# Performance work log

Measured on AMD Instinct MI355X. Metric: run time of the kernel, lower is better.

## Reference

```python
import jax, jax.numpy as jnp
import numpy as np

SEQ, BATCH, IN_DIM, NQ = 512, 512, 128, 8  # hidden_dim == n_qubits == 8


def setup_inputs() -> dict:
    key = jax.random.key(0)
    k1, k2, k3, k4 = jax.random.split(key, 4)
    inputs = jax.random.normal(k1, (SEQ, BATCH, IN_DIM), dtype=jnp.float32)
    h0 = jnp.zeros((BATCH, NQ), dtype=jnp.float32)
    c0 = jnp.zeros((BATCH, NQ), dtype=jnp.float32)
    D = IN_DIM + NQ
    # gate order: forget, input, update, output
    W = jax.random.normal(k2, (4, NQ, D), dtype=jnp.float32) / np.sqrt(D)
    b = jnp.zeros((4, NQ), dtype=jnp.float32)
    qp = jax.random.normal(k3, (4, NQ), dtype=jnp.float32)  # QLayer.params per gate
    return {"inputs": inputs, "h0": h0, "c0": c0, "W": W, "b": b, "qp": qp}


def _qlayer(z):
    # Analytic form of the RY/RY/CNOT-chain circuit: <Z_k> = prod_{j<=k} cos(theta_j)
    return jnp.cumprod(jnp.cos(z), axis=-1)


def reference(inputs, h0, c0, W, b, qp):
    def step(carry, x_t):
        h, c = carry
        comb = jnp.concatenate([x_t, h], axis=-1)            # (B, D)
        z = jnp.einsum('bd,gqd->bgq', comb, W) + b + qp      # (B, 4, NQ)
        q = _qlayer(z)
        f = jax.nn.sigmoid(q[:, 0])
        i = jax.nn.sigmoid(q[:, 1])
        g = jnp.tanh(q[:, 2])
        o = jax.nn.sigmoid(q[:, 3])
        c2 = f * c + i * g
        h2 = o * jnp.tanh(c2)
        return (h2, c2), h2

    (h_f, c_f), outputs = jax.lax.scan(step, (h0, c0), inputs)
    return outputs, h_f, c_f
```

## Files before the change

kernel.cpp:

```cpp
#include <hip/hip_runtime.h>


#define SEQ_LEN 512
#define BATCH_N 512
#define IN_DIMC 128
#define NQC 8
#define DTOT 136
#define GQ 32
#define M_ROWS (SEQ_LEN * BATCH_N)
#define OUT_MAIN (SEQ_LEN * BATCH_N * NQC)

__global__ __launch_bounds__(256) void zx_gemm(
    const float* __restrict__ X, const float* __restrict__ W,
    float* __restrict__ ZX)
{
    __shared__ __align__(16) float Wl[IN_DIMC * GQ];
    const int tid = threadIdx.x;

    #pragma unroll
    for (int i = 0; i < (IN_DIMC * GQ) / 256; ++i) {
        int idx = i * 256 + tid;
        int k  = idx >> 5;
        int gq = idx & 31;
        Wl[idx] = W[gq * DTOT + k];
    }
    __syncthreads();

    const float4* __restrict__ X4  = (const float4*)X;
    const float4* __restrict__ Wl4 = (const float4*)Wl;

    const int r0 = blockIdx.x * 512 + tid;
    const int r1 = r0 + 256;

    float4 accA[8], accB[8];
    #pragma unroll
    for (int q = 0; q < 8; ++q) {
        accA[q] = make_float4(0.f, 0.f, 0.f, 0.f);
        accB[q] = make_float4(0.f, 0.f, 0.f, 0.f);
    }

#define KSTEP(XA, XB, KIDX)                                                   \
    {                                                                         \
        _Pragma("unroll")                                                     \
        for (int q = 0; q < 8; ++q) {                                         \
            float4 w = Wl4[(KIDX) * 8 + q];                                   \
            accA[q].x = fmaf((XA), w.x, accA[q].x);                           \
            accA[q].y = fmaf((XA), w.y, accA[q].y);                           \
            accA[q].z = fmaf((XA), w.z, accA[q].z);                           \
            accA[q].w = fmaf((XA), w.w, accA[q].w);                           \
            accB[q].x = fmaf((XB), w.x, accB[q].x);                           \
            accB[q].y = fmaf((XB), w.y, accB[q].y);                           \
            accB[q].z = fmaf((XB), w.z, accB[q].z);                           \
            accB[q].w = fmaf((XB), w.w, accB[q].w);                           \
        }                                                                     \
    }

    #pragma unroll 2
    for (int k4 = 0; k4 < 32; ++k4) {
        float4 xa = X4[r0 * 32 + k4];
        float4 xb = X4[r1 * 32 + k4];
        KSTEP(xa.x, xb.x, k4 * 4 + 0)
        KSTEP(xa.y, xb.y, k4 * 4 + 1)
        KSTEP(xa.z, xb.z, k4 * 4 + 2)
        KSTEP(xa.w, xb.w, k4 * 4 + 3)
    }
#undef KSTEP

    float4* __restrict__ Z4 = (float4*)ZX;
    #pragma unroll
    for (int q = 0; q < 8; ++q) {
        Z4[r0 * 8 + q] = accA[q];
        Z4[r1 * 8 + q] = accB[q];
    }
}

__device__ __forceinline__ float fast_rcp(float x) {
    return __builtin_amdgcn_rcpf(x);
}
__device__ __forceinline__ float sigmoid_f(float x) {
    return fast_rcp(1.f + __expf(-x));
}
__device__ __forceinline__ float tanh_f(float x) {
    return fmaf(2.f, fast_rcp(1.f + __expf(-2.f * x)), -1.f);
}

__global__ __launch_bounds__(64) void qlstm_scan(
    const float* __restrict__ ZX, const float* __restrict__ W,
    const float* __restrict__ bv, const float* __restrict__ qp,
    const float* __restrict__ h0, const float* __restrict__ c0,
    float* __restrict__ out)
{
    const int tid = threadIdx.x;
    const int l32 = tid & 31;
    const int hw  = tid >> 5;
    const int qi  = l32 & 7;
    const int gq  = l32;
    const int row = blockIdx.x * 2 + hw;

    float wh[8];
    #pragma unroll
    for (int j = 0; j < 8; ++j) wh[j] = W[gq * DTOT + IN_DIMC + j];
    const float bias = bv[gq] + qp[gq];

    float hreg[8];
    #pragma unroll
    for (int j = 0; j < 8; ++j) hreg[j] = h0[row * 8 + j];
    float c = c0[row * 8 + qi];

    float zcur = ZX[(long)row * 32 + l32];

    float h2 = 0.f;
    for (int t = 0; t < SEQ_LEN; ++t) {
        const int tn = (t + 1 < SEQ_LEN) ? (t + 1) : (SEQ_LEN - 1);
        const float znext = ZX[((long)tn * BATCH_N + row) * 32 + l32];

        float z = zcur + bias;
        #pragma unroll
        for (int j = 0; j < 8; ++j) z = fmaf(hreg[j], wh[j], z);

        float p = __cosf(z);
        #pragma unroll
        for (int off = 1; off <= 4; off <<= 1) {
            int src = (qi >= off) ? (l32 - off) : l32;
            float pv = __shfl(p, src, 32);
            p = (qi >= off) ? p * pv : p;
        }

        float p0 = __shfl(p, qi,      32);
        float p1 = __shfl(p, qi + 8,  32);
        float p2 = __shfl(p, qi + 16, 32);
        float p3 = __shfl(p, qi + 24, 32);

        float fg = sigmoid_f(p0);
        float ig = sigmoid_f(p1);
        float gg = tanh_f(p2);
        float og = sigmoid_f(p3);

        float c2 = fmaf(fg, c, ig * gg);
        h2 = og * tanh_f(c2);
        c = c2;

        #pragma unroll
        for (int j = 0; j < 8; ++j) hreg[j] = __shfl(h2, j, 32);

        if (l32 < 8)
            out[((long)t * BATCH_N + row) * 8 + qi] = h2;

        zcur = znext;
    }

    if (l32 < 8) {
        out[OUT_MAIN + row * 8 + qi] = h2;
        out[OUT_MAIN + BATCH_N * NQC + row * 8 + qi] = c;
    }
}

extern "C" void kernel_launch(void* const* d_in, const int* in_sizes, int n_in,
                              void* d_out, int out_size, void* d_ws, size_t ws_size,
                              hipStream_t stream)
{
    const float* X  = (const float*)d_in[0];
    const float* h0 = (const float*)d_in[1];
    const float* c0 = (const float*)d_in[2];
    const float* W  = (const float*)d_in[3];
    const float* bv = (const float*)d_in[4];
    const float* qp = (const float*)d_in[5];
    float* out = (float*)d_out;
    float* ZX  = (float*)d_ws;

    zx_gemm<<<M_ROWS / 512, 256, 0, stream>>>(X, W, ZX);
    qlstm_scan<<<BATCH_N / 2, 64, 0, stream>>>(ZX, W, bv, qp, h0, c0, out);
}
```

Baseline: 420.4 us.

## Pack four rows per wave with DPP exchanges and fold bias into GEMM

The scan kernel now maps 16 lanes per batch row instead of 32, with each lane computing two gate pre-activations. It replaces ds_bpermute shuffles with DPP row rotations and shifts for the cumprod scan, the gate exchange and the h broadcast, and prefetches ZX two steps ahead. Bias plus qp is folded into the GEMM epilogue, and the GEMM loop gets explicit one-step X prefetch with unroll 1. The goal is to shorten the serial per-step latency chain and halve the number of waves. The cost is more math per lane and DPP direction handling (dirshr), which is fragile.

```diff
diff --git a/kernel.cpp b/kernel.cpp
--- a/kernel.cpp
+++ b/kernel.cpp
@@ -4,154 +4,208 @@
 #define SEQ_LEN 512
 #define BATCH_N 512
 #define IN_DIMC 128
-#define NQC 8
 #define DTOT 136
-#define GQ 32
-#define M_ROWS (SEQ_LEN * BATCH_N)
-#define OUT_MAIN (SEQ_LEN * BATCH_N * NQC)
+#define OUT_MAIN (SEQ_LEN * BATCH_N * 8)
 
 __global__ __launch_bounds__(256) void zx_gemm(
     const float* __restrict__ X, const float* __restrict__ W,
+    const float* __restrict__ bv, const float* __restrict__ qp,
     float* __restrict__ ZX)
 {
-    __shared__ __align__(16) float Wl[IN_DIMC * GQ];
+    __shared__ __align__(16) float Wl[IN_DIMC * 32];
     const int tid = threadIdx.x;
-
-    #pragma unroll
-    for (int i = 0; i < (IN_DIMC * GQ) / 256; ++i) {
+    #pragma unroll
+    for (int i = 0; i < 16; ++i) {
         int idx = i * 256 + tid;
-        int k  = idx >> 5;
-        int gq = idx & 31;
-        Wl[idx] = W[gq * DTOT + k];
+        Wl[idx] = W[(idx & 31) * DTOT + (idx >> 5)];
     }
     __syncthreads();
 
-    const float4* __restrict__ X4  = (const float4*)X;
-    const float4* __restrict__ Wl4 = (const float4*)Wl;
-
-    const int r0 = blockIdx.x * 512 + tid;
-    const int r1 = r0 + 256;
-
-    float4 accA[8], accB[8];
-    #pragma unroll
-    for (int q = 0; q < 8; ++q) {
-        accA[q] = make_float4(0.f, 0.f, 0.f, 0.f);
-        accB[q] = make_float4(0.f, 0.f, 0.f, 0.f);
-    }
-
-#define KSTEP(XA, XB, KIDX)                                                   \
-    {                                                                         \
-        _Pragma("unroll")                                                     \
-        for (int q = 0; q < 8; ++q) {                                         \
-            float4 w = Wl4[(KIDX) * 8 + q];                                   \
-            accA[q].x = fmaf((XA), w.x, accA[q].x);                           \
-            accA[q].y = fmaf((XA), w.y, accA[q].y);                           \
-            accA[q].z = fmaf((XA), w.z, accA[q].z);                           \
-            accA[q].w = fmaf((XA), w.w, accA[q].w);                           \
-            accB[q].x = fmaf((XB), w.x, accB[q].x);                           \
-            accB[q].y = fmaf((XB), w.y, accB[q].y);                           \
-            accB[q].z = fmaf((XB), w.z, accB[q].z);                           \
-            accB[q].w = fmaf((XB), w.w, accB[q].w);                           \
-        }                                                                     \
-    }
-
-    #pragma unroll 2
+    const long r0 = (long)blockIdx.x * 512 + tid;
+    const long r1 = r0 + 256;
+    const float4* __restrict__ X40 = (const float4*)X + r0 * 32;
+    const float4* __restrict__ X41 = (const float4*)X + r1 * 32;
+    const float4* __restrict__ W4  = (const float4*)Wl;
+
+    float4 a0[8], a1[8];
+    #pragma unroll
+    for (int qq = 0; qq < 8; ++qq) {
+        a0[qq] = make_float4(0.f, 0.f, 0.f, 0.f);
+        a1[qq] = make_float4(0.f, 0.f, 0.f, 0.f);
+    }
+
+    float4 xa = X40[0], xb = X41[0];
+    #pragma unroll 1
     for (int k4 = 0; k4 < 32; ++k4) {
-        float4 xa = X4[r0 * 32 + k4];
-        float4 xb = X4[r1 * 32 + k4];
-        KSTEP(xa.x, xb.x, k4 * 4 + 0)
-        KSTEP(xa.y, xb.y, k4 * 4 + 1)
-        KSTEP(xa.z, xb.z, k4 * 4 + 2)
-        KSTEP(xa.w, xb.w, k4 * 4 + 3)
-    }
-#undef KSTEP
+        float4 xan = xa, xbn = xb;
+        if (k4 < 31) { xan = X40[k4 + 1]; xbn = X41[k4 + 1]; }
+        #pragma unroll
+        for (int c = 0; c < 4; ++c) {
+            const float va = (c==0)?xa.x:(c==1)?xa.y:(c==2)?xa.z:xa.w;
+            const float vb = (c==0)?xb.x:(c==1)?xb.y:(c==2)?xb.z:xb.w;
+            #pragma unroll
+            for (int qq = 0; qq < 8; ++qq) {
+                const float4 w = W4[(k4 * 4 + c) * 8 + qq];
+                a0[qq].x = fmaf(va, w.x, a0[qq].x);
+                a0[qq].y = fmaf(va, w.y, a0[qq].y);
+                a0[qq].z = fmaf(va, w.z, a0[qq].z);
+                a0[qq].w = fmaf(va, w.w, a0[qq].w);
+                a1[qq].x = fmaf(vb, w.x, a1[qq].x);
+                a1[qq].y = fmaf(vb, w.y, a1[qq].y);
+                a1[qq].z = fmaf(vb, w.z, a1[qq].z);
+                a1[qq].w = fmaf(vb, w.w, a1[qq].w);
+            }
+        }
+        xa = xan; xb = xbn;
+    }
 
     float4* __restrict__ Z4 = (float4*)ZX;
     #pragma unroll
-    for (int q = 0; q < 8; ++q) {
-        Z4[r0 * 8 + q] = accA[q];
-        Z4[r1 * 8 + q] = accB[q];
+    for (int qq = 0; qq < 8; ++qq) {
+        const int g0 = qq * 4;
+        float4 o0 = a0[qq], o1 = a1[qq];
+        const float b0 = bv[g0+0] + qp[g0+0];
+        const float b1_ = bv[g0+1] + qp[g0+1];
+        const float b2 = bv[g0+2] + qp[g0+2];
+        const float b3 = bv[g0+3] + qp[g0+3];
+        o0.x += b0; o0.y += b1_; o0.z += b2; o0.w += b3;
+        o1.x += b0; o1.y += b1_; o1.z += b2; o1.w += b3;
+        Z4[r0 * 8 + qq] = o0;
+        Z4[r1 * 8 + qq] = o1;
     }
 }
 
-__device__ __forceinline__ float fast_rcp(float x) {
-    return __builtin_amdgcn_rcpf(x);
-}
-__device__ __forceinline__ float sigmoid_f(float x) {
-    return fast_rcp(1.f + __expf(-x));
-}
-__device__ __forceinline__ float tanh_f(float x) {
-    return fmaf(2.f, fast_rcp(1.f + __expf(-2.f * x)), -1.f);
-}
+#define DPP_F(x, ctrl) \
+    __builtin_bit_cast(float, __builtin_amdgcn_update_dpp( \
+        0, __builtin_bit_cast(int, (x)), (ctrl), 0xF, 0xF, true))
 
 __global__ __launch_bounds__(64) void qlstm_scan(
     const float* __restrict__ ZX, const float* __restrict__ W,
-    const float* __restrict__ bv, const float* __restrict__ qp,
     const float* __restrict__ h0, const float* __restrict__ c0,
     float* __restrict__ out)
 {
-    const int tid = threadIdx.x;
-    const int l32 = tid & 31;
-    const int hw  = tid >> 5;
-    const int qi  = l32 & 7;
-    const int gq  = l32;
-    const int row = blockIdx.x * 2 + hw;
-
-    float wh[8];
-    #pragma unroll
-    for (int j = 0; j < 8; ++j) wh[j] = W[gq * DTOT + IN_DIMC + j];
-    const float bias = bv[gq] + qp[gq];
-
-    float hreg[8];
-    #pragma unroll
-    for (int j = 0; j < 8; ++j) hreg[j] = h0[row * 8 + j];
-    float c = c0[row * 8 + qi];
-
-    float zcur = ZX[(long)row * 32 + l32];
-
-    float h2 = 0.f;
+    const int l   = threadIdx.x;
+    const int l16 = l & 15;
+    const int q   = l & 7;
+    const int hB  = l16 >> 3;
+    const int row = blockIdx.x * 4 + (l >> 4);
+    const int gq0 = l16;
+    const int gq1 = 16 + l16;
+
+    const float qf = (float)q;
+    int jmap[8];
+    jmap[0] = q;
+    jmap[1] = (int)DPP_F(qf, 0x121);
+    jmap[2] = (int)DPP_F(qf, 0x122);
+    jmap[3] = (int)DPP_F(qf, 0x123);
+    jmap[4] = (int)DPP_F(qf, 0x124);
+    jmap[5] = (int)DPP_F(qf, 0x125);
+    jmap[6] = (int)DPP_F(qf, 0x126);
+    jmap[7] = (int)DPP_F(qf, 0x127);
+
+    const bool dirshr = ((int)DPP_F(qf, 0x111) == q - 1);
+
+    float wh0[8], wh1[8], hror[8];
+    #pragma unroll
+    for (int r = 0; r < 8; ++r) {
+        wh0[r]  = W[gq0 * DTOT + IN_DIMC + jmap[r]];
+        wh1[r]  = W[gq1 * DTOT + IN_DIMC + jmap[r]];
+        hror[r] = h0[row * 8 + jmap[r]];
+    }
+    float c = c0[row * 8 + q];
+
+    const bool ge1 = (q >= 1), ge2 = (q >= 2), ge4 = (q >= 4);
+    const bool isT = (hB == 0);
+    const float m1 = isT ? -2.f : -1.f;
+    const float A1 = isT ?  2.f :  1.f;
+    const float B1 = isT ? -1.f :  0.f;
+
+    float zb0  = ZX[(long)row * 32 + l16];
+    float zb1  = ZX[(long)row * 32 + 16 + l16];
+    float zn10 = ZX[((long)BATCH_N + row) * 32 + l16];
+    float zn11 = ZX[((long)BATCH_N + row) * 32 + 16 + l16];
+
+    float hlast = 0.f;
     for (int t = 0; t < SEQ_LEN; ++t) {
-        const int tn = (t + 1 < SEQ_LEN) ? (t + 1) : (SEQ_LEN - 1);
-        const float znext = ZX[((long)tn * BATCH_N + row) * 32 + l32];
-
-        float z = zcur + bias;
-        #pragma unroll
-        for (int j = 0; j < 8; ++j) z = fmaf(hreg[j], wh[j], z);
-
-        float p = __cosf(z);
-        #pragma unroll
-        for (int off = 1; off <= 4; off <<= 1) {
-            int src = (qi >= off) ? (l32 - off) : l32;
-            float pv = __shfl(p, src, 32);
-            p = (qi >= off) ? p * pv : p;
-        }
-
-        float p0 = __shfl(p, qi,      32);
-        float p1 = __shfl(p, qi + 8,  32);
-        float p2 = __shfl(p, qi + 16, 32);
-        float p3 = __shfl(p, qi + 24, 32);
-
-        float fg = sigmoid_f(p0);
-        float ig = sigmoid_f(p1);
-        float gg = tanh_f(p2);
-        float og = sigmoid_f(p3);
-
-        float c2 = fmaf(fg, c, ig * gg);
-        h2 = og * tanh_f(c2);
+        const long tp = (t + 2 < SEQ_LEN) ? (t + 2) : (SEQ_LEN - 1);
+        const float zn20 = ZX[(tp * BATCH_N + row) * 32 + l16];
+        const float zn21 = ZX[(tp * BATCH_N + row) * 32 + 16 + l16];
+
+        float s0a = fmaf(hror[0], wh0[0], zb0);
+        s0a = fmaf(hror[1], wh0[1], s0a);
+        s0a = fmaf(hror[2], wh0[2], s0a);
+        s0a = fmaf(hror[3], wh0[3], s0a);
+        float s0b = hror[4] * wh0[4];
+        s0b = fmaf(hror[5], wh0[5], s0b);
+        s0b = fmaf(hror[6], wh0[6], s0b);
+        s0b = fmaf(hror[7], wh0[7], s0b);
+        const float z0 = s0a + s0b;
+
+        float s1a = fmaf(hror[0], wh1[0], zb1);
+        s1a = fmaf(hror[1], wh1[1], s1a);
+        s1a = fmaf(hror[2], wh1[2], s1a);
+        s1a = fmaf(hror[3], wh1[3], s1a);
+        float s1b = hror[4] * wh1[4];
+        s1b = fmaf(hror[5], wh1[5], s1b);
+        s1b = fmaf(hror[6], wh1[6], s1b);
+        s1b = fmaf(hror[7], wh1[7], s1b);
+        const float z1 = s1a + s1b;
+
+        float p0 = __cosf(z0), p1 = __cosf(z1);
+
+        float ashr = p0, ashl = p0, bshr = p1, bshl = p1;
+        { float v = DPP_F(ashr, 0x111); ashr *= ge1 ? v : 1.f; }
+        { float v = DPP_F(bshr, 0x111); bshr *= ge1 ? v : 1.f; }
+        { float v = DPP_F(ashl, 0x101); ashl *= ge1 ? v : 1.f; }
+        { float v = DPP_F(bshl, 0x101); bshl *= ge1 ? v : 1.f; }
+        { float v = DPP_F(ashr, 0x112); ashr *= ge2 ? v : 1.f; }
+        { float v = DPP_F(bshr, 0x112); bshr *= ge2 ? v : 1.f; }
+        { float v = DPP_F(ashl, 0x102); ashl *= ge2 ? v : 1.f; }
+        { float v = DPP_F(bshl, 0x102); bshl *= ge2 ? v : 1.f; }
+        { float v = DPP_F(ashr, 0x114); ashr *= ge4 ? v : 1.f; }
+        { float v = DPP_F(bshr, 0x114); bshr *= ge4 ? v : 1.f; }
+        { float v = DPP_F(ashl, 0x104); ashl *= ge4 ? v : 1.f; }
+        { float v = DPP_F(bshl, 0x104); bshl *= ge4 ? v : 1.f; }
+        p0 = dirshr ? ashr : ashl;
+        p1 = dirshr ? bshr : bshl;
+
+        const float act0 = __builtin_amdgcn_rcpf(1.f + __expf(-p0));
+        const float act1 = fmaf(
+            __builtin_amdgcn_rcpf(1.f + __expf(p1 * m1)), A1, B1);
+
+        const float oth0 = DPP_F(act0, 0x128);
+        const float oth1 = DPP_F(act1, 0x128);
+
+        const float f_ = hB ? oth0 : act0;
+        const float i_ = hB ? act0 : oth0;
+        const float g_ = hB ? oth1 : act1;
+        const float o_ = hB ? act1 : oth1;
+
+        const float c2 = fmaf(f_, c, i_ * g_);
+        const float th = fmaf(
+            __builtin_amdgcn_rcpf(1.f + __expf(-2.f * c2)), 2.f, -1.f);
+        const float h2 = o_ * th;
         c = c2;
-
-        #pragma unroll
-        for (int j = 0; j < 8; ++j) hreg[j] = __shfl(h2, j, 32);
-
-        if (l32 < 8)
-            out[((long)t * BATCH_N + row) * 8 + qi] = h2;
-
-        zcur = znext;
-    }
-
-    if (l32 < 8) {
-        out[OUT_MAIN + row * 8 + qi] = h2;
-        out[OUT_MAIN + BATCH_N * NQC + row * 8 + qi] = c;
+        hlast = h2;
+
+        if (l16 < 8) out[((long)t * BATCH_N + row) * 8 + q] = h2;
+
+        hror[0] = h2;
+        hror[1] = DPP_F(h2, 0x121);
+        hror[2] = DPP_F(h2, 0x122);
+        hror[3] = DPP_F(h2, 0x123);
+        hror[4] = DPP_F(h2, 0x124);
+        hror[5] = DPP_F(h2, 0x125);
+        hror[6] = DPP_F(h2, 0x126);
+        hror[7] = DPP_F(h2, 0x127);
+
+        zb0 = zn10; zb1 = zn11;
+        zn10 = zn20; zn11 = zn21;
+    }
+
+    if (l16 < 8) {
+        out[OUT_MAIN + row * 8 + q] = hlast;
+        out[OUT_MAIN + BATCH_N * 8 + row * 8 + q] = c;
     }
 }
 
@@ -168,6 +222,6 @@
     float* out = (float*)d_out;
     float* ZX  = (float*)d_ws;
 
-    zx_gemm<<<M_ROWS / 512, 256, 0, stream>>>(X, W, ZX);
-    qlstm_scan<<<BATCH_N / 2, 64, 0, stream>>>(ZX, W, bv, qp, h0, c0, out);
+    zx_gemm<<<(SEQ_LEN * BATCH_N) / 512, 256, 0, stream>>>(X, W, bv, qp, ZX);
+    qlstm_scan<<<BATCH_N / 4, 64, 0, stream>>>(ZX, W, h0, c0, out);
 }
```

Result: faster. 389.6 us (-7.3%).
